# Performance work log

Measured on AMD Instinct MI355X. Metric: run time of the kernel, lower is better.

Reference implementation:

```python
import jax, jax.numpy as jnp
import numpy as np

BSZ, SEQ, D, NHEAD, NLAYER, DFF, NQ = 4, 48, 256, 2, 2, 2048, 512
LN_EPS = 1e-5
NEG = jnp.float32(-1e30)


def _layernorm(x, w, b):
    m = jnp.mean(x, axis=-1, keepdims=True)
    v = jnp.mean((x - m) ** 2, axis=-1, keepdims=True)
    return (x - m) / jnp.sqrt(v + LN_EPS) * w + b


def _span_max(x):
    # Cumulative span max: span[b,s,e] = max(x[b,s:e+1]) for e>=s, else 0.
    B, S, H = x.shape
    padded = jnp.concatenate([x, jnp.full((B, S, H), NEG, x.dtype)], axis=1)  # [B,2S,H]

    def step(tmp, i):
        shifted = jax.lax.dynamic_slice(padded, (0, i, 0), (B, S, H))  # x shifted left by i, padded with -inf
        tmp = jnp.maximum(tmp, shifted)  # tmp[b,s] = max(x[b,s:s+i+1])
        return tmp, tmp

    _, ys = jax.lax.scan(step, jnp.full((B, S, H), NEG, x.dtype), jnp.arange(S))
    # ys: [width, B, start, H]; span[b,s,e] = ys[e-s, b, s]
    si = jnp.arange(S)[:, None]
    ei = jnp.arange(S)[None, :]
    w = jnp.clip(ei - si, 0, S - 1)
    span = ys[w, :, jnp.broadcast_to(si, (S, S))]  # [S_start, S_end, B, H]
    span = jnp.where((ei >= si)[:, :, None, None], span, 0.0)
    return span.transpose(2, 0, 1, 3)  # [B,S,S,H]


def _mha(x, wi, bi, wo, bo, kpm):
    # x: [B,T,D]; kpm: [B,T] bool, True = masked key
    B, T, Dm = x.shape
    hd = Dm // NHEAD
    qkv = x @ wi.T + bi
    q, k, v = jnp.split(qkv, 3, axis=-1)
    rs = lambda a: a.reshape(B, T, NHEAD, hd).transpose(0, 2, 1, 3)
    q, k, v = rs(q), rs(k), rs(v)
    scores = jnp.einsum('bhqd,bhkd->bhqk', q, k) * (1.0 / np.sqrt(hd))
    scores = jnp.where(kpm[:, None, None, :], -1e9, scores)
    p = jax.nn.softmax(scores, axis=-1)
    o = jnp.einsum('bhqk,bhkd->bhqd', p, v).transpose(0, 2, 1, 3).reshape(B, T, Dm)
    return o @ wo.T + bo


def _encoder(x, kpm, iw, ib, ow, ob, l1w, l1b, l2w, l2b, f1w, f1b, f2w, f2b, fw, fb):
    # Post-norm torch TransformerEncoder (eval mode, relu, no dropout)
    for l in range(NLAYER):
        a = _mha(x, iw[l], ib[l], ow[l], ob[l], kpm)
        x = _layernorm(x + a, l1w[l], l1b[l])
        f = jax.nn.relu(x @ f1w[l].T + f1b[l]) @ f2w[l].T + f2b[l]
        x = _layernorm(x + f, l2w[l], l2b[l])
    return _layernorm(x, fw, fb)


def _forward(enc, iw, ib, ow, ob, l1w, l1b, l2w, l2b, f1w, f1b, f2w, f2b, fw, fb, s1, e1, qb, s2, e2):
    span = _span_max(enc)  # [B,S,S,D]
    idx = jnp.arange(SEQ)
    kpm2d = idx[None, :] < idx[:, None]  # [start,end]: True where end < start
    kpm = jnp.broadcast_to(kpm2d.reshape(1, SEQ * SEQ), (BSZ, SEQ * SEQ))
    out = _encoder(span.reshape(BSZ, SEQ * SEQ, D), kpm, iw, ib, ow, ob, l1w, l1b, l2w, l2b, f1w, f1b, f2w, f2b, fw, fb)
    out = out.reshape(BSZ, SEQ, SEQ, D)
    res1 = out[qb, s1, e1]
    res2 = out[qb, s2, e2]
    return res1, res2


def setup_inputs() -> dict:
    key = jax.random.key(0)
    ks = jax.random.split(key, 16)
    sc = 0.02
    enc = jax.random.normal(ks[0], (BSZ, SEQ, D), jnp.float32)
    inp = {
        'encoded_input': enc,
        'in_proj_w': jax.random.normal(ks[1], (NLAYER, 3 * D, D), jnp.float32) * sc,
        'in_proj_b': jnp.zeros((NLAYER, 3 * D), jnp.float32),
        'out_proj_w': jax.random.normal(ks[2], (NLAYER, D, D), jnp.float32) * sc,
        'out_proj_b': jnp.zeros((NLAYER, D), jnp.float32),
        'ln1_w': jnp.ones((NLAYER, D), jnp.float32),
        'ln1_b': jnp.zeros((NLAYER, D), jnp.float32),
        'ln2_w': jnp.ones((NLAYER, D), jnp.float32),
        'ln2_b': jnp.zeros((NLAYER, D), jnp.float32),
        'ff1_w': jax.random.normal(ks[3], (NLAYER, DFF, D), jnp.float32) * sc,
        'ff1_b': jnp.zeros((NLAYER, DFF), jnp.float32),
        'ff2_w': jax.random.normal(ks[4], (NLAYER, D, DFF), jnp.float32) * sc,
        'ff2_b': jnp.zeros((NLAYER, D), jnp.float32),
        'fln_w': jnp.ones((D,), jnp.float32),
        'fln_b': jnp.zeros((D,), jnp.float32),
    }
    s1 = jax.random.randint(ks[5], (NQ,), 0, SEQ)
    e1 = jnp.minimum(s1 + jax.random.randint(ks[6], (NQ,), 0, SEQ), SEQ - 1)
    s2 = jax.random.randint(ks[7], (NQ,), 0, SEQ)
    e2 = jnp.minimum(s2 + jax.random.randint(ks[8], (NQ,), 0, SEQ), SEQ - 1)
    inp['start_ids_1'] = s1
    inp['end_ids_1'] = e1
    inp['query_batch_idx'] = jax.random.randint(ks[9], (NQ,), 0, BSZ)
    inp['start_ids_2'] = s2
    inp['end_ids_2'] = e2
    return inp


def reference(encoded_input, in_proj_w, in_proj_b, out_proj_w, out_proj_b, ln1_w, ln1_b, ln2_w, ln2_b, ff1_w, ff1_b, ff2_w, ff2_b, fln_w, fln_b, start_ids_1, end_ids_1, query_batch_idx, start_ids_2, end_ids_2):
    return _forward(encoded_input, in_proj_w, in_proj_b, out_proj_w, out_proj_b, ln1_w, ln1_b, ln2_w, ln2_b, ff1_w, ff1_b, ff2_w, ff2_b, fln_w, fln_b, start_ids_1, end_ids_1, query_batch_idx, start_ids_2, end_ids_2)
```

## Files before the change

kernel.cpp:

```cpp
#include <hip/hip_runtime.h>
#include <hip/hip_bf16.h>

#define BSZ 4
#define SEQ 48
#define DMODEL 256
#define NHEAD 2
#define HD 128
#define NLAYERS 2
#define DFF_C 2048
#define NQ_C 512
#define NV 1176
#define NTOT (BSZ * NV)
#define NVP 1216
#define KSPLIT 5
#define FSPLIT 4
#define OSPLIT 2
#define SCALE 0.088388347648318447f

typedef unsigned short u16;
typedef __attribute__((ext_vector_type(8))) short bf16x8;
typedef __attribute__((ext_vector_type(4))) float f32x4;

__device__ inline u16 f2b(float f) {
    __hip_bfloat16 h = __float2bfloat16(f);
    return *reinterpret_cast<u16*>(&h);
}
__device__ inline void storeval(float* p, float v) { *p = v; }
__device__ inline void storeval(u16* p, float v) { *p = f2b(v); }

__global__ __launch_bounds__(256) void castspan_kernel(
    const float* __restrict__ iw, const float* __restrict__ ow,
    const float* __restrict__ f1w, const float* __restrict__ f2w,
    u16* __restrict__ iwb, u16* __restrict__ owb,
    u16* __restrict__ f1wb, u16* __restrict__ f2wb,
    const float* __restrict__ enc, float* __restrict__ X,
    u16* __restrict__ Xb, u16* __restrict__ VT) {
    int bid = blockIdx.x;
    if (bid < 2560) {
        int i = bid * 256 + threadIdx.x;
        const float* src;
        u16* dst;
        int off;
        if (i < 98304)       { src = iw;  dst = iwb;  off = i; }
        else if (i < 131072) { src = ow;  dst = owb;  off = i - 98304; }
        else if (i < 393216) { src = f1w; dst = f1wb; off = i - 131072; }
        else                 { src = f2w; dst = f2wb; off = i - 393216; }
        float4 v = *(const float4*)(src + (size_t)off * 4);
        *(ushort4*)(dst + (size_t)off * 4) =
            make_ushort4(f2b(v.x), f2b(v.y), f2b(v.z), f2b(v.w));
    } else if (bid < 2752) {
        int sb = bid - 2560;
        int i = sb % SEQ, b = sb / SEQ, h = threadIdx.x;
        int tb = i * SEQ - (i * (i - 1)) / 2 - i;
        float run = -1e30f;
        for (int j = i; j < SEQ; ++j) {
            run = fmaxf(run, enc[((size_t)b * SEQ + j) * DMODEL + h]);
            size_t idx = ((size_t)b * NV + tb + j) * DMODEL + h;
            X[idx] = run;
            Xb[idx] = f2b(run);
        }
    } else {
        int i = (bid - 2752) * 256 + threadIdx.x;
        int row = i / 20, off = i % 20;
        ((unsigned int*)VT)[(size_t)row * (NVP / 2) + (NV / 2) + off] = 0u;
    }
}

template <typename OutT, bool RELU, bool VOUT>
__global__ __launch_bounds__(256) void mm_kernel(
    const u16* __restrict__ A, const u16* __restrict__ W,
    const float* __restrict__ bias, const float* __restrict__ Res,
    OutT* __restrict__ C, u16* __restrict__ VTout,
    int N, int K, int lda, int ldw, int ldc,
    float alpha, int WV, int KC, int splitRows) {
    __shared__ u16 As[64][72];
    __shared__ u16 Ws[64][72];
    const float4 fz = make_float4(0.f, 0.f, 0.f, 0.f);
    int ks = blockIdx.z;
    int kb = ks * KC, ke = min(K, kb + KC);
    if (splitRows) C += (size_t)ks * splitRows * ldc;
    int p0 = blockIdx.x * 64, n0 = blockIdx.y * 64;
    int tid = threadIdx.x, lane = tid & 63, w = tid >> 6;
    int col_l = lane & 15, quad = lane >> 4;
    f32x4 acc[4] = {};
    for (int k0 = kb; k0 < ke; k0 += 64) {
        int r = tid >> 2, seg = (tid & 3) * 16;
        {
            int gn = n0 + r;
            const u16* ap = A + (size_t)gn * lda + k0 + seg;
            float4 a0 = fz, a1 = fz;
            if (gn < N) { a0 = *(const float4*)ap; a1 = *(const float4*)(ap + 8); }
            *(float4*)&As[r][seg] = a0;
            *(float4*)&As[r][seg + 8] = a1;
        }
        {
            int gp = p0 + r;
            const u16* wp = W + (size_t)gp * ldw + k0 + seg;
            float4 w0 = fz, w1 = fz;
            if (gp < WV) { w0 = *(const float4*)wp; w1 = *(const float4*)(wp + 8); }
            *(float4*)&Ws[r][seg] = w0;
            *(float4*)&Ws[r][seg + 8] = w1;
        }
        __syncthreads();
        bf16x8 a0 = *(const bf16x8*)&As[w * 16 + col_l][quad * 8];
        bf16x8 a1 = *(const bf16x8*)&As[w * 16 + col_l][32 + quad * 8];
#pragma unroll
        for (int c = 0; c < 4; ++c) {
            bf16x8 b0 = *(const bf16x8*)&Ws[c * 16 + col_l][quad * 8];
            bf16x8 b1 = *(const bf16x8*)&Ws[c * 16 + col_l][32 + quad * 8];
            acc[c] = __builtin_amdgcn_mfma_f32_16x16x32_bf16(a0, b0, acc[c], 0, 0, 0);
            acc[c] = __builtin_amdgcn_mfma_f32_16x16x32_bf16(a1, b1, acc[c], 0, 0, 0);
        }
        __syncthreads();
    }
    int row0 = n0 + w * 16 + quad * 4;
#pragma unroll
    for (int c = 0; c < 4; ++c) {
        int col = p0 + c * 16 + col_l;
        float bv = bias ? bias[col] : 0.f;
        float vv[4];
#pragma unroll
        for (int reg = 0; reg < 4; ++reg) {
            int row = row0 + reg;
            float v = acc[c][reg] * alpha + bv;
            if (Res && row < N) v += Res[(size_t)row * ldc + col];
            if (RELU) v = fmaxf(v, 0.f);
            vv[reg] = v;
        }
        if (VOUT && col >= 2 * DMODEL) {
            if (row0 < N) {
                int b = row0 / NV, t = row0 - b * NV;
                int d = col - 2 * DMODEL;
                *(ushort4*)(VTout + ((size_t)(b * 2 + (d >> 7)) * HD + (d & 127)) * NVP + t) =
                    make_ushort4(f2b(vv[0]), f2b(vv[1]), f2b(vv[2]), f2b(vv[3]));
            }
        } else {
#pragma unroll
            for (int reg = 0; reg < 4; ++reg)
                if (row0 + reg < N)
                    storeval(&C[(size_t)(row0 + reg) * ldc + col], vv[reg]);
        }
    }
}

template <typename OutT, bool RELU>
__global__ __launch_bounds__(256) void mmw_kernel(
    const u16* __restrict__ A, const u16* __restrict__ W,
    const float* __restrict__ bias,
    OutT* __restrict__ C, int N, int K, int lda, int ldw, int ldc,
    int WV, int KC, int splitRows) {
    __shared__ u16 As[64][72];
    __shared__ u16 Ws[128][72];
    const float4 fz = make_float4(0.f, 0.f, 0.f, 0.f);
    int ks = blockIdx.z;
    int kb = ks * KC, ke = min(K, kb + KC);
    if (splitRows) C += (size_t)ks * splitRows * ldc;
    int p0 = blockIdx.x * 128, n0 = blockIdx.y * 64;
    int tid = threadIdx.x, lane = tid & 63, w = tid >> 6;
    int col_l = lane & 15, quad = lane >> 4;
    f32x4 acc[8] = {};
    for (int k0 = kb; k0 < ke; k0 += 64) {
        {
            int r = tid >> 2, seg = (tid & 3) * 16;
            int gn = n0 + r;
            const u16* ap = A + (size_t)gn * lda + k0 + seg;
            float4 a0 = fz, a1 = fz;
            if (gn < N) { a0 = *(const float4*)ap; a1 = *(const float4*)(ap + 8); }
            *(float4*)&As[r][seg] = a0;
            *(float4*)&As[r][seg + 8] = a1;
        }
        {
            int r2 = tid >> 1, seg2 = (tid & 1) * 32;
            int gp = p0 + r2;
            const u16* wp = W + (size_t)gp * ldw + k0 + seg2;
#pragma unroll
            for (int j = 0; j < 4; ++j) {
                float4 wv = fz;
                if (gp < WV) wv = *(const float4*)(wp + j * 8);
                *(float4*)&Ws[r2][seg2 + j * 8] = wv;
            }
        }
        __syncthreads();
        bf16x8 a0 = *(const bf16x8*)&As[w * 16 + col_l][quad * 8];
        bf16x8 a1 = *(const bf16x8*)&As[w * 16 + col_l][32 + quad * 8];
#pragma unroll
        for (int c = 0; c < 8; ++c) {
            bf16x8 b0 = *(const bf16x8*)&Ws[c * 16 + col_l][quad * 8];
            bf16x8 b1 = *(const bf16x8*)&Ws[c * 16 + col_l][32 + quad * 8];
            acc[c] = __builtin_amdgcn_mfma_f32_16x16x32_bf16(a0, b0, acc[c], 0, 0, 0);
            acc[c] = __builtin_amdgcn_mfma_f32_16x16x32_bf16(a1, b1, acc[c], 0, 0, 0);
        }
        __syncthreads();
    }
#pragma unroll
    for (int c = 0; c < 8; ++c) {
        int col = p0 + c * 16 + col_l;
        float bv = bias ? bias[col] : 0.f;
#pragma unroll
        for (int reg = 0; reg < 4; ++reg) {
            int row = n0 + w * 16 + quad * 4 + reg;
            if (row < N) {
                float v = acc[c][reg] + bv;
                if (RELU) v = fmaxf(v, 0.f);
                storeval(&C[(size_t)row * ldc + col], v);
            }
        }
    }
}

__global__ __launch_bounds__(256) void flash_kernel(const u16* __restrict__ QKVb,
                                                    const u16* __restrict__ VT,
                                                    float* __restrict__ Opart,
                                                    float* __restrict__ ML) {
    __shared__ u16 Ks[64][136];
    __shared__ u16 Vt[128][72];
    __shared__ u16 Ps[4][16][72];
    const float4 fz = make_float4(0.f, 0.f, 0.f, 0.f);
    int tid = threadIdx.x, lane = tid & 63, w = tid >> 6;
    int col_l = lane & 15, quad = lane >> 4;
    int bh = blockIdx.y, b = bh >> 1, h = bh & 1;
    int ks = blockIdx.z;
    int t0 = ks * 4, tcnt = min(4, 19 - t0);
    size_t rb = (size_t)b * NV;
    int q0 = blockIdx.x * 64, wq0 = q0 + w * 16;

    float4 qv[4];
    {
        int qrow = wq0 + col_l;
        if (qrow < NV) {
            const u16* qp = QKVb + (rb + qrow) * 768 + h * HD + quad * 8;
#pragma unroll
            for (int kf = 0; kf < 4; ++kf) qv[kf] = *(const float4*)(qp + kf * 32);
        } else {
#pragma unroll
            for (int kf = 0; kf < 4; ++kf) qv[kf] = fz;
        }
    }

    f32x4 oacc[8] = {};
    float m_run[4], l_run[4];
#pragma unroll
    for (int r = 0; r < 4; ++r) { m_run[r] = -1e30f; l_run[r] = 0.f; }

    for (int it = 0; it < tcnt; ++it) {
        int kt = (t0 + it) * 64;
        {
            int r = tid >> 2, seg = (tid & 3) * 32;
            int key = kt + r;
            const u16* kp = QKVb + (rb + key) * 768 + DMODEL + h * HD + seg;
#pragma unroll
            for (int t4 = 0; t4 < 4; ++t4) {
                float4 v = fz;
                if (key < NV) v = *(const float4*)(kp + t4 * 8);
                *(float4*)&Ks[r][seg + t4 * 8] = v;
            }
        }
        {
            int d = tid >> 1, half = (tid & 1) * 32;
            const u16* vp = VT + ((size_t)bh * HD + d) * NVP + kt + half;
#pragma unroll
            for (int t4 = 0; t4 < 4; ++t4)
                *(float4*)&Vt[d][half + t4 * 8] = *(const float4*)(vp + t4 * 8);
        }
        __syncthreads();

        f32x4 s[4] = {};
#pragma unroll
        for (int c = 0; c < 4; ++c)
#pragma unroll
            for (int kf = 0; kf < 4; ++kf) {
                bf16x8 kfr = *(const bf16x8*)&Ks[c * 16 + col_l][kf * 32 + quad * 8];
                s[c] = __builtin_amdgcn_mfma_f32_16x16x32_bf16(
                    *(const bf16x8*)&qv[kf], kfr, s[c], 0, 0, 0);
            }

        float pv[4][4];
#pragma unroll
        for (int c = 0; c < 4; ++c) {
            bool kvalid = (kt + c * 16 + col_l) < NV;
#pragma unroll
            for (int r = 0; r < 4; ++r)
                pv[c][r] = kvalid ? s[c][r] * SCALE : -1e30f;
        }
        float mxv[4];
        int need = 0;
#pragma unroll
        for (int r = 0; r < 4; ++r) {
            float mx = fmaxf(fmaxf(pv[0][r], pv[1][r]), fmaxf(pv[2][r], pv[3][r]));
#pragma unroll
            for (int off = 1; off < 16; off <<= 1)
                mx = fmaxf(mx, __shfl_xor(mx, off));
            mxv[r] = mx;
            need |= (mx > m_run[r] + 8.f) ? 1 : 0;
        }
        if (__any(need)) {
#pragma unroll
            for (int r = 0; r < 4; ++r) {
                float mn = fmaxf(m_run[r], mxv[r]);
                float al = __expf(m_run[r] - mn);
                m_run[r] = mn;
                l_run[r] *= al;
#pragma unroll
                for (int ct = 0; ct < 8; ++ct) oacc[ct][r] *= al;
            }
        }
#pragma unroll
        for (int r = 0; r < 4; ++r) {
            float sum = 0.f;
#pragma unroll
            for (int c = 0; c < 4; ++c) {
                float pp = __expf(pv[c][r] - m_run[r]);
                pv[c][r] = pp;
                sum += pp;
            }
#pragma unroll
            for (int off = 1; off < 16; off <<= 1) sum += __shfl_xor(sum, off);
            l_run[r] += sum;
        }

#pragma unroll
        for (int c = 0; c < 4; ++c)
#pragma unroll
            for (int r = 0; r < 4; ++r)
                Ps[w][quad * 4 + r][c * 16 + col_l] = f2b(pv[c][r]);
        bf16x8 pf0 = *(const bf16x8*)&Ps[w][col_l][quad * 8];
        bf16x8 pf1 = *(const bf16x8*)&Ps[w][col_l][32 + quad * 8];
#pragma unroll
        for (int ct = 0; ct < 8; ++ct) {
            bf16x8 v0 = *(const bf16x8*)&Vt[ct * 16 + col_l][quad * 8];
            bf16x8 v1 = *(const bf16x8*)&Vt[ct * 16 + col_l][32 + quad * 8];
            oacc[ct] = __builtin_amdgcn_mfma_f32_16x16x32_bf16(pf0, v0, oacc[ct], 0, 0, 0);
            oacc[ct] = __builtin_amdgcn_mfma_f32_16x16x32_bf16(pf1, v1, oacc[ct], 0, 0, 0);
        }
        __syncthreads();
    }

    size_t slab = (size_t)(ks * 8 + bh) * NVP;
#pragma unroll
    for (int ct = 0; ct < 8; ++ct)
#pragma unroll
        for (int r = 0; r < 4; ++r) {
            int row = wq0 + quad * 4 + r;
            Opart[(slab + row) * HD + ct * 16 + col_l] = oacc[ct][r];
        }
    if (col_l == 0) {
#pragma unroll
        for (int r = 0; r < 4; ++r) {
            int row = wq0 + quad * 4 + r;
            ML[(slab + row) * 2 + 0] = m_run[r];
            ML[(slab + row) * 2 + 1] = l_run[r];
        }
    }
}

__global__ __launch_bounds__(256) void comb_kernel(const float* __restrict__ Opart,
                                                   const float* __restrict__ ML,
                                                   u16* __restrict__ Obuf) {
    int bh = blockIdx.y, b = bh >> 1, h = bh & 1;
    int tid = threadIdx.x;
    int row = blockIdx.x * 2 + (tid >> 7);
    int d = tid & 127;
    if (row >= NV) return;
    float m[KSPLIT], l[KSPLIT];
#pragma unroll
    for (int i = 0; i < KSPLIT; ++i) {
        size_t mb = ((size_t)(i * 8 + bh) * NVP + row) * 2;
        m[i] = ML[mb];
        l[i] = ML[mb + 1];
    }
    float M = m[0];
#pragma unroll
    for (int i = 1; i < KSPLIT; ++i) M = fmaxf(M, m[i]);
    float wsum = 0.f, o = 0.f;
#pragma unroll
    for (int i = 0; i < KSPLIT; ++i) {
        float wi = __expf(m[i] - M);
        wsum += l[i] * wi;
        o += Opart[((size_t)(i * 8 + bh) * NVP + row) * HD + d] * wi;
    }
    Obuf[((size_t)b * NV + row) * DMODEL + h * HD + d] = f2b(o / wsum);
}

template <int NSLAB>
__global__ __launch_bounds__(256) void redln_kernel(const float* __restrict__ Xres,
                                                    const float* __restrict__ P,
                                                    const float* __restrict__ cbias,
                                                    const float* __restrict__ w,
                                                    const float* __restrict__ bb,
                                                    float* __restrict__ Y,
                                                    u16* __restrict__ Yb) {
    int wv = threadIdx.x >> 6, lane = threadIdx.x & 63;
    int r = blockIdx.x * 4 + wv;
    size_t base = (size_t)r * DMODEL + lane * 4;
    float4 v = *(const float4*)(Xres + base);
    float4 c4 = *(const float4*)(cbias + lane * 4);
    v.x += c4.x; v.y += c4.y; v.z += c4.z; v.w += c4.w;
#pragma unroll
    for (int z = 0; z < NSLAB; ++z) {
        float4 p4 = *(const float4*)(P + (size_t)z * NTOT * DMODEL + base);
        v.x += p4.x; v.y += p4.y; v.z += p4.z; v.w += p4.w;
    }
    float s1 = v.x + v.y + v.z + v.w;
    float s2 = v.x * v.x + v.y * v.y + v.z * v.z + v.w * v.w;
#pragma unroll
    for (int off = 32; off > 0; off >>= 1) {
        s1 += __shfl_xor(s1, off);
        s2 += __shfl_xor(s2, off);
    }
    float mean = s1 * (1.f / DMODEL);
    float var = s2 * (1.f / DMODEL) - mean * mean;
    float rstd = rsqrtf(var + 1e-5f);
    float4 w4 = *(const float4*)(w + lane * 4);
    float4 b4 = *(const float4*)(bb + lane * 4);
    float o0 = (v.x - mean) * rstd * w4.x + b4.x;
    float o1 = (v.y - mean) * rstd * w4.y + b4.y;
    float o2 = (v.z - mean) * rstd * w4.z + b4.z;
    float o3 = (v.w - mean) * rstd * w4.w + b4.w;
    *(float4*)(Y + base) = make_float4(o0, o1, o2, o3);
    *(ushort4*)(Yb + base) = make_ushort4(f2b(o0), f2b(o1), f2b(o2), f2b(o3));
}

__global__ __launch_bounds__(64) void gatherln2_kernel(const float* __restrict__ Xres,
                                                       const float* __restrict__ P,
                                                       const float* __restrict__ cbias,
                                                       const float* __restrict__ w2,
                                                       const float* __restrict__ b2,
                                                       const float* __restrict__ fw,
                                                       const float* __restrict__ fb,
                                                       const int* __restrict__ s1,
                                                       const int* __restrict__ e1,
                                                       const int* __restrict__ qb,
                                                       const int* __restrict__ s2,
                                                       const int* __restrict__ e2,
                                                       float* __restrict__ out) {
    int q = blockIdx.x, which = blockIdx.y, lane = threadIdx.x;
    int s = which ? s2[q] : s1[q];
    int e = which ? e2[q] : e1[q];
    int b = qb[q];
    int t = s * SEQ - (s * (s - 1)) / 2 + (e - s);
    if (t < 0) t = 0;
    if (t >= NV) t = NV - 1;
    size_t base = ((size_t)b * NV + t) * DMODEL + lane * 4;
    float4 v = *(const float4*)(Xres + base);
    float4 c4 = *(const float4*)(cbias + lane * 4);
    v.x += c4.x; v.y += c4.y; v.z += c4.z; v.w += c4.w;
#pragma unroll
    for (int z = 0; z < FSPLIT; ++z) {
        float4 p4 = *(const float4*)(P + (size_t)z * NTOT * DMODEL + base);
        v.x += p4.x; v.y += p4.y; v.z += p4.z; v.w += p4.w;
    }
    float s1v = v.x + v.y + v.z + v.w;
    float s2v = v.x * v.x + v.y * v.y + v.z * v.z + v.w * v.w;
#pragma unroll
    for (int off = 32; off > 0; off >>= 1) {
        s1v += __shfl_xor(s1v, off);
        s2v += __shfl_xor(s2v, off);
    }
    float mean = s1v * (1.f / DMODEL);
    float var = s2v * (1.f / DMODEL) - mean * mean;
    float rstd = rsqrtf(var + 1e-5f);
    float4 w4 = *(const float4*)(w2 + lane * 4);
    float4 b4 = *(const float4*)(b2 + lane * 4);
    float o0 = (v.x - mean) * rstd * w4.x + b4.x;
    float o1 = (v.y - mean) * rstd * w4.y + b4.y;
    float o2 = (v.z - mean) * rstd * w4.z + b4.z;
    float o3 = (v.w - mean) * rstd * w4.w + b4.w;
    float t1 = o0 + o1 + o2 + o3;
    float t2 = o0 * o0 + o1 * o1 + o2 * o2 + o3 * o3;
#pragma unroll
    for (int off = 32; off > 0; off >>= 1) {
        t1 += __shfl_xor(t1, off);
        t2 += __shfl_xor(t2, off);
    }
    float mean2 = t1 * (1.f / DMODEL);
    float var2 = t2 * (1.f / DMODEL) - mean2 * mean2;
    float rstd2 = rsqrtf(var2 + 1e-5f);
    float4 fw4 = *(const float4*)(fw + lane * 4);
    float4 fb4 = *(const float4*)(fb + lane * 4);
    float r0 = (o0 - mean2) * rstd2 * fw4.x + fb4.x;
    float r1 = (o1 - mean2) * rstd2 * fw4.y + fb4.y;
    float r2 = (o2 - mean2) * rstd2 * fw4.z + fb4.z;
    float r3 = (o3 - mean2) * rstd2 * fw4.w + fb4.w;
    *(float4*)(out + ((size_t)which * NQ_C + q) * DMODEL + lane * 4) =
        make_float4(r0, r1, r2, r3);
}

extern "C" void kernel_launch(void* const* d_in, const int* in_sizes, int n_in,
                              void* d_out, int out_size, void* d_ws, size_t ws_size,
                              hipStream_t stream) {
    const float* enc = (const float*)d_in[0];
    const float* iw  = (const float*)d_in[1];
    const float* ib  = (const float*)d_in[2];
    const float* ow  = (const float*)d_in[3];
    const float* ob  = (const float*)d_in[4];
    const float* l1w = (const float*)d_in[5];
    const float* l1b = (const float*)d_in[6];
    const float* l2w = (const float*)d_in[7];
    const float* l2b = (const float*)d_in[8];
    const float* f1w = (const float*)d_in[9];
    const float* f1b = (const float*)d_in[10];
    const float* f2w = (const float*)d_in[11];
    const float* f2b_ = (const float*)d_in[12];
    const float* flw = (const float*)d_in[13];
    const float* flb = (const float*)d_in[14];
    const int* s1 = (const int*)d_in[15];
    const int* e1 = (const int*)d_in[16];
    const int* qb = (const int*)d_in[17];
    const int* s2 = (const int*)d_in[18];
    const int* e2 = (const int*)d_in[19];
    float* out = (float*)d_out;

    char* p = (char*)d_ws;
    float* X     = (float*)p;  p += (size_t)NTOT * DMODEL * 4;
    u16* Xb      = (u16*)p;    p += (size_t)NTOT * DMODEL * 2;
    u16* Obuf    = (u16*)p;    p += (size_t)NTOT * DMODEL * 2;
    u16* QKVb    = (u16*)p;    p += (size_t)NTOT * 3 * DMODEL * 2;
    u16* VT      = (u16*)p;    p += (size_t)8 * HD * NVP * 2;
    float* ML    = (float*)p;  p += (size_t)KSPLIT * 8 * NVP * 2 * 4;
    float* Opart = (float*)p;  p += (size_t)KSPLIT * 8 * NVP * HD * 4;
    float* Pbuf  = (float*)p;  p += (size_t)FSPLIT * NTOT * DMODEL * 4;
    u16* wb      = (u16*)p;
    u16* F1b     = (u16*)Opart;

    u16* iwb  = wb;
    u16* owb  = iwb + 2 * 3 * DMODEL * DMODEL;
    u16* f1wb = owb + 2 * DMODEL * DMODEL;
    u16* f2wb = f1wb + 2 * DFF_C * DMODEL;

    castspan_kernel<<<dim3(2832), 256, 0, stream>>>(iw, ow, f1w, f2w,
                                                    iwb, owb, f1wb, f2wb,
                                                    enc, X, Xb, VT);

    for (int l = 0; l < NLAYERS; ++l) {
        mm_kernel<u16, false, true><<<dim3(12, 74, 1), 256, 0, stream>>>(
            Xb, iwb + (size_t)l * 3 * DMODEL * DMODEL, ib + (size_t)l * 3 * DMODEL,
            nullptr, QKVb, VT, NTOT, DMODEL, DMODEL, DMODEL, 3 * DMODEL, 1.f,
            3 * DMODEL, DMODEL, 0);
        flash_kernel<<<dim3(19, 8, KSPLIT), 256, 0, stream>>>(QKVb, VT, Opart, ML);
        comb_kernel<<<dim3(588, 8), 256, 0, stream>>>(Opart, ML, Obuf);
        mm_kernel<float, false, false><<<dim3(4, 74, OSPLIT), 256, 0, stream>>>(
            Obuf, owb + (size_t)l * DMODEL * DMODEL, nullptr, nullptr, Pbuf,
            nullptr, NTOT, DMODEL, DMODEL, DMODEL, DMODEL, 1.f, DMODEL,
            DMODEL / OSPLIT, NTOT);
        redln_kernel<OSPLIT><<<dim3(NTOT / 4), 256, 0, stream>>>(
            X, Pbuf, ob + (size_t)l * DMODEL,
            l1w + (size_t)l * DMODEL, l1b + (size_t)l * DMODEL, X, Xb);
        mmw_kernel<u16, true><<<dim3(16, 74, 1), 256, 0, stream>>>(
            Xb, f1wb + (size_t)l * DFF_C * DMODEL, f1b + (size_t)l * DFF_C,
            F1b, NTOT, DMODEL, DMODEL, DMODEL, DFF_C, DFF_C, DMODEL, 0);
        mmw_kernel<float, false><<<dim3(2, 74, FSPLIT), 256, 0, stream>>>(
            F1b, f2wb + (size_t)l * DMODEL * DFF_C, nullptr, Pbuf,
            NTOT, DFF_C, DFF_C, DFF_C, DMODEL, DMODEL, DFF_C / FSPLIT, NTOT);
        if (l < NLAYERS - 1) {
            redln_kernel<FSPLIT><<<dim3(NTOT / 4), 256, 0, stream>>>(
                X, Pbuf, f2b_ + (size_t)l * DMODEL,
                l2w + (size_t)l * DMODEL, l2b + (size_t)l * DMODEL, X, Xb);
        } else {
            gatherln2_kernel<<<dim3(NQ_C, 2), 64, 0, stream>>>(
                X, Pbuf, f2b_ + (size_t)l * DMODEL,
                l2w + (size_t)l * DMODEL, l2b + (size_t)l * DMODEL,
                flw, flb, s1, e1, qb, s2, e2, out);
        }
    }
}
```

Measured before the change: 299.1 us.

## Fuse split-K attention combine into flash kernel via last-block atomic counter

Removes the separate combine kernel: each flash block increments a per-(query tile, batch-head) atomic counter, and the last split-K block to finish merges the partial outputs and max/sum stats into the bf16 output. The merge uses vectorised float4 reads. The QK buffer also narrows its row stride from 768 to 512 because V is written only in transposed form. This saves a kernel launch and a pass over the partials, in exchange for threadfences, an atomic per block, and a serial tail of combine work on the last block.

```diff
diff --git a/kernel.cpp b/kernel.cpp
--- a/kernel.cpp
+++ b/kernel.cpp
@@ -15,6 +15,7 @@
 #define KSPLIT 5
 #define FSPLIT 4
 #define OSPLIT 2
+#define LDQK 512
 #define SCALE 0.088388347648318447f
 
 typedef unsigned short u16;
@@ -34,7 +35,7 @@
     u16* __restrict__ iwb, u16* __restrict__ owb,
     u16* __restrict__ f1wb, u16* __restrict__ f2wb,
     const float* __restrict__ enc, float* __restrict__ X,
-    u16* __restrict__ Xb, u16* __restrict__ VT) {
+    u16* __restrict__ Xb, u16* __restrict__ VT, int* __restrict__ cnt) {
     int bid = blockIdx.x;
     if (bid < 2560) {
         int i = bid * 256 + threadIdx.x;
@@ -59,10 +60,12 @@
             X[idx] = run;
             Xb[idx] = f2b(run);
         }
-    } else {
+    } else if (bid < 2832) {
         int i = (bid - 2752) * 256 + threadIdx.x;
         int row = i / 20, off = i % 20;
         ((unsigned int*)VT)[(size_t)row * (NVP / 2) + (NV / 2) + off] = 0u;
+    } else {
+        if (threadIdx.x < 19 * 8) cnt[threadIdx.x] = 0;
     }
 }
 
@@ -208,13 +211,16 @@
     }
 }
 
-__global__ __launch_bounds__(256) void flash_kernel(const u16* __restrict__ QKVb,
+__global__ __launch_bounds__(256) void flash_kernel(const u16* __restrict__ QKb,
                                                     const u16* __restrict__ VT,
                                                     float* __restrict__ Opart,
-                                                    float* __restrict__ ML) {
+                                                    float* __restrict__ ML,
+                                                    u16* __restrict__ Obuf,
+                                                    int* __restrict__ cnt) {
     __shared__ u16 Ks[64][136];
     __shared__ u16 Vt[128][72];
     __shared__ u16 Ps[4][16][72];
+    __shared__ int amLast;
     const float4 fz = make_float4(0.f, 0.f, 0.f, 0.f);
     int tid = threadIdx.x, lane = tid & 63, w = tid >> 6;
     int col_l = lane & 15, quad = lane >> 4;
@@ -228,7 +234,7 @@
     {
         int qrow = wq0 + col_l;
         if (qrow < NV) {
-            const u16* qp = QKVb + (rb + qrow) * 768 + h * HD + quad * 8;
+            const u16* qp = QKb + (rb + qrow) * LDQK + h * HD + quad * 8;
 #pragma unroll
             for (int kf = 0; kf < 4; ++kf) qv[kf] = *(const float4*)(qp + kf * 32);
         } else {
@@ -247,7 +253,7 @@
         {
             int r = tid >> 2, seg = (tid & 3) * 32;
             int key = kt + r;
-            const u16* kp = QKVb + (rb + key) * 768 + DMODEL + h * HD + seg;
+            const u16* kp = QKb + (rb + key) * LDQK + DMODEL + h * HD + seg;
 #pragma unroll
             for (int t4 = 0; t4 < 4; ++t4) {
                 float4 v = fz;
@@ -351,34 +357,61 @@
             ML[(slab + row) * 2 + 1] = l_run[r];
         }
     }
-}
-
-__global__ __launch_bounds__(256) void comb_kernel(const float* __restrict__ Opart,
-                                                   const float* __restrict__ ML,
-                                                   u16* __restrict__ Obuf) {
-    int bh = blockIdx.y, b = bh >> 1, h = bh & 1;
-    int tid = threadIdx.x;
-    int row = blockIdx.x * 2 + (tid >> 7);
-    int d = tid & 127;
-    if (row >= NV) return;
-    float m[KSPLIT], l[KSPLIT];
-#pragma unroll
-    for (int i = 0; i < KSPLIT; ++i) {
-        size_t mb = ((size_t)(i * 8 + bh) * NVP + row) * 2;
-        m[i] = ML[mb];
-        l[i] = ML[mb + 1];
-    }
-    float M = m[0];
-#pragma unroll
-    for (int i = 1; i < KSPLIT; ++i) M = fmaxf(M, m[i]);
-    float wsum = 0.f, o = 0.f;
-#pragma unroll
-    for (int i = 0; i < KSPLIT; ++i) {
-        float wi = __expf(m[i] - M);
-        wsum += l[i] * wi;
-        o += Opart[((size_t)(i * 8 + bh) * NVP + row) * HD + d] * wi;
-    }
-    Obuf[((size_t)b * NV + row) * DMODEL + h * HD + d] = f2b(o / wsum);
+
+    __threadfence();
+    __syncthreads();
+    if (tid == 0) {
+        int old = atomicAdd(&cnt[blockIdx.x * 8 + bh], 1);
+        amLast = (old == KSPLIT - 1);
+        if (old == KSPLIT - 1) cnt[blockIdx.x * 8 + bh] = 0;
+    }
+    __syncthreads();
+    if (!amLast) return;
+    __threadfence();
+
+    float* wls = (float*)Ks;
+    if (tid < 64) {
+        int row = q0 + tid;
+        if (row < NV) {
+            float m[KSPLIT], l[KSPLIT];
+#pragma unroll
+            for (int i = 0; i < KSPLIT; ++i) {
+                const float* mp = ML + ((size_t)(i * 8 + bh) * NVP + row) * 2;
+                m[i] = mp[0];
+                l[i] = mp[1];
+            }
+            float M = m[0];
+#pragma unroll
+            for (int i = 1; i < KSPLIT; ++i) M = fmaxf(M, m[i]);
+            float ws = 0.f;
+#pragma unroll
+            for (int i = 0; i < KSPLIT; ++i) {
+                float wi = __expf(m[i] - M);
+                wls[tid * 6 + i] = wi;
+                ws += l[i] * wi;
+            }
+            wls[tid * 6 + 5] = ws;
+        }
+    }
+    __syncthreads();
+#pragma unroll
+    for (int j = 0; j < 8; ++j) {
+        int idx = j * 256 + tid;
+        int ri = idx >> 5, dg = idx & 31;
+        int row = q0 + ri;
+        if (row >= NV) continue;
+        int d = dg * 4;
+        float o0 = 0.f, o1 = 0.f, o2 = 0.f, o3 = 0.f;
+#pragma unroll
+        for (int i = 0; i < KSPLIT; ++i) {
+            float4 p4 = *(const float4*)(Opart + ((size_t)(i * 8 + bh) * NVP + row) * HD + d);
+            float wi = wls[ri * 6 + i];
+            o0 += p4.x * wi; o1 += p4.y * wi; o2 += p4.z * wi; o3 += p4.w * wi;
+        }
+        float ws = wls[ri * 6 + 5];
+        *(ushort4*)(Obuf + ((size_t)b * NV + row) * DMODEL + h * HD + d) =
+            make_ushort4(f2b(o0 / ws), f2b(o1 / ws), f2b(o2 / ws), f2b(o3 / ws));
+    }
 }
 
 template <int NSLAB>
@@ -514,7 +547,7 @@
     float* X     = (float*)p;  p += (size_t)NTOT * DMODEL * 4;
     u16* Xb      = (u16*)p;    p += (size_t)NTOT * DMODEL * 2;
     u16* Obuf    = (u16*)p;    p += (size_t)NTOT * DMODEL * 2;
-    u16* QKVb    = (u16*)p;    p += (size_t)NTOT * 3 * DMODEL * 2;
+    u16* QKb     = (u16*)p;    p += (size_t)NTOT * LDQK * 2;
     u16* VT      = (u16*)p;    p += (size_t)8 * HD * NVP * 2;
     float* ML    = (float*)p;  p += (size_t)KSPLIT * 8 * NVP * 2 * 4;
     float* Opart = (float*)p;  p += (size_t)KSPLIT * 8 * NVP * HD * 4;
@@ -526,18 +559,19 @@
     u16* owb  = iwb + 2 * 3 * DMODEL * DMODEL;
     u16* f1wb = owb + 2 * DMODEL * DMODEL;
     u16* f2wb = f1wb + 2 * DFF_C * DMODEL;
-
-    castspan_kernel<<<dim3(2832), 256, 0, stream>>>(iw, ow, f1w, f2w,
+    int* cnt  = (int*)(f2wb + 2 * DMODEL * DFF_C);
+
+    castspan_kernel<<<dim3(2833), 256, 0, stream>>>(iw, ow, f1w, f2w,
                                                     iwb, owb, f1wb, f2wb,
-                                                    enc, X, Xb, VT);
+                                                    enc, X, Xb, VT, cnt);
 
     for (int l = 0; l < NLAYERS; ++l) {
         mm_kernel<u16, false, true><<<dim3(12, 74, 1), 256, 0, stream>>>(
             Xb, iwb + (size_t)l * 3 * DMODEL * DMODEL, ib + (size_t)l * 3 * DMODEL,
-            nullptr, QKVb, VT, NTOT, DMODEL, DMODEL, DMODEL, 3 * DMODEL, 1.f,
+            nullptr, QKb, VT, NTOT, DMODEL, DMODEL, DMODEL, LDQK, 1.f,
             3 * DMODEL, DMODEL, 0);
-        flash_kernel<<<dim3(19, 8, KSPLIT), 256, 0, stream>>>(QKVb, VT, Opart, ML);
-        comb_kernel<<<dim3(588, 8), 256, 0, stream>>>(Opart, ML, Obuf);
+        flash_kernel<<<dim3(19, 8, KSPLIT), 256, 0, stream>>>(QKb, VT, Opart, ML,
+                                                              Obuf, cnt);
         mm_kernel<float, false, false><<<dim3(4, 74, OSPLIT), 256, 0, stream>>>(
             Obuf, owb + (size_t)l * DMODEL * DMODEL, nullptr, nullptr, Pbuf,
             nullptr, NTOT, DMODEL, DMODEL, DMODEL, DMODEL, 1.f, DMODEL,
```

New measurement: 507.5 us. 1.7x slower.
